# Kernel optimization log

Measured on AMD Instinct MI355X. Metric: run time of the kernel, lower is better.

## Reference

```python
import jax, jax.numpy as jnp
import numpy as np

B, T, D = 2, 2048, 2048
H, DK = 16, 96
DV = 192                 # head_v_dim = head_dim * expand_v (expand_v=2)
KEY_DIM = H * DK         # 1536 = 0.75*D
VAL_DIM = H * DV         # 3072 = 1.5*D
KS = 4                   # short-conv kernel size
EPS = 1e-6


def setup_inputs() -> dict:
    key = jax.random.key(0)
    ks = jax.random.split(key, 16)
    nrm = lambda k, shape, s: jax.random.normal(k, shape, jnp.float32) * s
    # dt_bias init as in the torch module
    dt_min, dt_max = 1e-3, 1e-1
    dt = jnp.exp(jax.random.uniform(ks[12], (H,), jnp.float32)
                 * (np.log(dt_max) - np.log(dt_min)) + np.log(dt_min))
    dt_bias = dt + jnp.log(-jnp.expm1(-dt))
    return {
        'x': nrm(ks[0], (B, T, D), 1.0),
        'Wq': nrm(ks[1], (D, KEY_DIM), D ** -0.5),
        'Wk': nrm(ks[2], (D, KEY_DIM), D ** -0.5),
        'Wv': nrm(ks[3], (D, VAL_DIM), D ** -0.5),
        'Wb': nrm(ks[4], (D, H), D ** -0.5),
        'Wa': nrm(ks[5], (D, H), D ** -0.5),
        'Wg': nrm(ks[6], (D, VAL_DIM), D ** -0.5),
        'Wo': nrm(ks[7], (VAL_DIM, D), VAL_DIM ** -0.5),
        'conv_q_w': nrm(ks[8], (KEY_DIM, KS), KS ** -0.5),
        'conv_k_w': nrm(ks[9], (KEY_DIM, KS), KS ** -0.5),
        'conv_v_w': nrm(ks[10], (VAL_DIM, KS), KS ** -0.5),
        'A_log': jnp.log(jax.random.uniform(ks[11], (H,), jnp.float32, 1e-4, 16.0)),
        'dt_bias': dt_bias,
        'o_norm_weight': jnp.ones((DV,), jnp.float32),
    }


def _causal_depthwise_conv(x, w):
    # x: (B, T, C), w: (C, KS). Depthwise causal conv + SiLU.
    xp = jnp.pad(x, ((0, 0), (KS - 1, 0), (0, 0)))
    y = sum(xp[:, j:j + T, :] * w[:, j] for j in range(KS))
    return jax.nn.silu(y)


def _gated_delta_scan(q, k, v, g, beta):
    # q,k: (B,T,H,DK)  v: (B,T,H,DV)  g,beta: (B,T,H)
    def step(S, inp):
        q_t, k_t, v_t, g_t, b_t = inp          # (B,H,DK),(B,H,DK),(B,H,DV),(B,H),(B,H)
        alpha = jnp.exp(g_t)                   # (B,H)
        retrieved = jnp.einsum('bhk,bhkv->bhv', k_t, S)
        error = v_t - retrieved                # (B,H,DV)
        S = alpha[:, :, None, None] * S + b_t[:, :, None, None] * (
            k_t[:, :, :, None] * error[:, :, None, :])
        o_t = jnp.einsum('bhk,bhkv->bhv', q_t, S)
        return S, o_t

    tm = lambda a: jnp.swapaxes(a, 0, 1)       # time-major
    S0 = jnp.zeros((B, H, DK, DV), jnp.float32)
    _, o = jax.lax.scan(step, S0, (tm(q), tm(k), tm(v), tm(g), tm(beta)))
    return jnp.swapaxes(o, 0, 1)               # (B,T,H,DV)


def reference(x, Wq, Wk, Wv, Wb, Wa, Wg, Wo,
              conv_q_w, conv_k_w, conv_v_w, A_log, dt_bias, o_norm_weight):
    # projections + causal depthwise short conv + SiLU
    q = _causal_depthwise_conv(x @ Wq, conv_q_w).reshape(B, T, H, DK)
    k = _causal_depthwise_conv(x @ Wk, conv_k_w).reshape(B, T, H, DK)
    v = _causal_depthwise_conv(x @ Wv, conv_v_w).reshape(B, T, H, DV)

    beta = jax.nn.sigmoid(x @ Wb)                                   # (B,T,H)
    g = -jnp.exp(A_log) * jax.nn.softplus(x @ Wa + dt_bias)         # (B,T,H)

    # qk L2 normalization (use_qk_l2norm_in_kernel=True path)
    q = q * jax.lax.rsqrt(jnp.sum(q * q, -1, keepdims=True) + 1e-12)
    k = k * jax.lax.rsqrt(jnp.sum(k * k, -1, keepdims=True) + 1e-12)

    o = _gated_delta_scan(q, k, v, g, beta)                         # (B,T,H,DV)

    # gated RMSNorm over head_v_dim
    g_out = (x @ Wg).reshape(B, T, H, DV)
    rms = jax.lax.rsqrt(jnp.mean(o * o, -1, keepdims=True) + EPS)
    o = (o * rms) * o_norm_weight * jax.nn.sigmoid(g_out)

    return o.reshape(B, T, VAL_DIM) @ Wo                            # (B,T,D)
```

## Files before the change

kernel.cpp:

```cpp
#include <hip/hip_runtime.h>

#define B_ 2
#define T_ 2048
#define D_ 2048
#define H_ 16
#define DK_ 96
#define DV_ 192
#define KEYD 1536
#define VALD 3072
#define NPROJ 9216
#define PQK 6144
#define KS_ 4
#define C_ 64
#define NC_ 32

typedef unsigned short u16;
typedef unsigned int u32;
typedef __bf16 bf16x8 __attribute__((ext_vector_type(8)));
typedef float f32x4 __attribute__((ext_vector_type(4)));

__device__ __forceinline__ u16 f2bf(float f) {
  unsigned u = __float_as_uint(f);
  u += 0x7FFF + ((u >> 16) & 1);
  return (u16)(u >> 16);
}
__device__ __forceinline__ float bf2f(u16 v) { return __uint_as_float((unsigned)v << 16); }
__device__ __forceinline__ float bflo(u32 w) { return __uint_as_float(w << 16); }
__device__ __forceinline__ float bfhi(u32 w) { return __uint_as_float(w & 0xFFFF0000u); }

__device__ __forceinline__ void gll16(const void* g, void* lds) {
  __builtin_amdgcn_global_load_lds(
      (const __attribute__((address_space(1))) void*)g,
      (__attribute__((address_space(3))) void*)lds, 16, 0, 0);
}

__global__ __launch_bounds__(256) void cast_x(const float* __restrict__ in,
                                              u16* __restrict__ out, int n4) {
  int i = blockIdx.x * 256 + threadIdx.x;
  if (i < n4) {
    float4 v = reinterpret_cast<const float4*>(in)[i];
    ushort4 o;
    o.x = f2bf(v.x); o.y = f2bf(v.y); o.z = f2bf(v.z); o.w = f2bf(v.w);
    reinterpret_cast<ushort4*>(out)[i] = o;
  }
}

__global__ __launch_bounds__(256) void transpose_cast(const float* __restrict__ src,
                                                      u16* __restrict__ dst, int R, int C) {
  __shared__ float tile[32][33];
  int tx = threadIdx.x & 31, ty = threadIdx.x >> 5;
  int c0 = blockIdx.x * 32, r0 = blockIdx.y * 32;
#pragma unroll
  for (int j = 0; j < 4; ++j)
    tile[ty + j * 8][tx] = src[(size_t)(r0 + ty + j * 8) * C + c0 + tx];
  __syncthreads();
#pragma unroll
  for (int j = 0; j < 4; ++j)
    dst[(size_t)(c0 + ty + j * 8) * R + r0 + tx] = f2bf(tile[tx][ty + j * 8]);
}

template <int OUT16>
__global__ __launch_bounds__(512, 2) void gemm256(const u16* __restrict__ A,
    const u16* __restrict__ BT, u16* __restrict__ C0, u16* __restrict__ C1,
    float* __restrict__ Cf, int M, int N, int K, int nsplit, int s0, int s1) {
  __shared__ u16 LA[2][256 * 64];
  __shared__ u16 LB[2][256 * 64];
  const int tid = threadIdx.x, wave = tid >> 6, lane = tid & 63;
  const int l15 = lane & 15, l16 = lane >> 4, x7 = l15 & 7;
  const int wr = wave >> 2, wc = wave & 3;
  const int m0 = blockIdx.y * 256, n0 = blockIdx.x * 256;
  const int r8 = lane >> 3;
  const int csrc = ((lane & 7) ^ r8) << 3;
  const int NKT = K >> 6;
  f32x4 acc[8][4] = {};

#define STG_A(p, kt, half) { \
    const u16* As_ = A + (size_t)m0 * K + (size_t)(kt) * 64; \
    _Pragma("unroll") \
    for (int g = 0; g < 2; ++g) { \
      int rowb = g * 128 + (half) * 64 + wave * 8; \
      gll16(As_ + (size_t)(rowb + r8) * K + csrc, (char*)&LA[p][0] + rowb * 128); \
    } \
  }
#define STG_B(p, kt) { \
    const u16* Bs_ = BT + (size_t)n0 * K + (size_t)(kt) * 64; \
    _Pragma("unroll") \
    for (int j = 0; j < 4; ++j) { \
      int rowb = j * 64 + wave * 8; \
      gll16(Bs_ + (size_t)(rowb + r8) * K + csrc, (char*)&LB[p][0] + rowb * 128); \
    } \
  }

#define LDA8(p, mh, dst) { \
    _Pragma("unroll") \
    for (int mi = 0; mi < 4; ++mi) \
      _Pragma("unroll") \
      for (int kk = 0; kk < 2; ++kk) { \
        int row = wr * 128 + (mh) * 64 + mi * 16 + l15; \
        dst[mi * 2 + kk] = *(const bf16x8*)((const char*)&LA[p][0] + row * 128 + (((kk * 4 + l16) ^ x7) << 4)); \
      } \
  }
#define LDB4(p, nh, dst) { \
    _Pragma("unroll") \
    for (int ni = 0; ni < 2; ++ni) \
      _Pragma("unroll") \
      for (int kk = 0; kk < 2; ++kk) { \
        int row = wc * 64 + (nh) * 32 + ni * 16 + l15; \
        dst[ni * 2 + kk] = *(const bf16x8*)((const char*)&LB[p][0] + row * 128 + (((kk * 4 + l16) ^ x7) << 4)); \
      } \
  }

#define MMQ(AF, BF, mbase, nbase) { \
    __builtin_amdgcn_s_setprio(1); \
    _Pragma("unroll") \
    for (int mi = 0; mi < 4; ++mi) \
      _Pragma("unroll") \
      for (int ni = 0; ni < 2; ++ni) \
        _Pragma("unroll") \
        for (int kk = 0; kk < 2; ++kk) \
          acc[(mbase) + mi][(nbase) + ni] = __builtin_amdgcn_mfma_f32_16x16x32_bf16( \
              AF[mi * 2 + kk], BF[ni * 2 + kk], acc[(mbase) + mi][(nbase) + ni], 0, 0, 0); \
    __builtin_amdgcn_s_setprio(0); \
  }

#define BARR() __builtin_amdgcn_s_barrier()
#define LGKM0() { asm volatile("s_waitcnt lgkmcnt(0)" ::: "memory"); __builtin_amdgcn_sched_barrier(0); }

  STG_A(0, 0, 0); STG_A(0, 0, 1); STG_B(0, 0);
  if (NKT > 1) {
    STG_A(1, 1, 0); STG_A(1, 1, 1); STG_B(1, 1);
    asm volatile("s_waitcnt vmcnt(8)" ::: "memory");
  } else {
    asm volatile("s_waitcnt vmcnt(0)" ::: "memory");
  }
  BARR();

  bf16x8 afA[8], afB[8], bf0[4], bf1[4];
  for (int c = 0; c < NKT; ++c) {
    const int p = c & 1;
    const bool stg = (c + 2 < NKT);
    LDA8(p, 0, afA); LDB4(p, 0, bf0);
    BARR();
    LGKM0();
    MMQ(afA, bf0, 0, 0);
    BARR();
    LDB4(p, 1, bf1);
    if (stg) STG_A(p, c + 2, 0);
    BARR();
    LGKM0();
    MMQ(afA, bf1, 0, 2);
    BARR();
    LDA8(p, 1, afB);
    if (stg) STG_B(p, c + 2);
    BARR();
    LGKM0();
    MMQ(afB, bf1, 4, 2);
    BARR();
    if (stg) {
      STG_A(p, c + 2, 1);
      asm volatile("s_waitcnt vmcnt(8)" ::: "memory");
    } else if (c + 1 < NKT) {
      asm volatile("s_waitcnt vmcnt(0)" ::: "memory");
    }
    BARR();
    MMQ(afB, bf0, 4, 0);
    BARR();
  }

#pragma unroll
  for (int mi = 0; mi < 8; ++mi)
#pragma unroll
    for (int ni = 0; ni < 4; ++ni)
#pragma unroll
      for (int j = 0; j < 4; ++j) {
        int row = m0 + wr * 128 + mi * 16 + l16 * 4 + j;
        int col = n0 + wc * 64 + ni * 16 + l15;
        float v = acc[mi][ni][j];
        if (OUT16) {
          if (col < nsplit) C0[(size_t)row * s0 + col] = f2bf(v);
          else              C1[(size_t)row * s1 + col - nsplit] = f2bf(v);
        } else {
          Cf[(size_t)row * N + col] = v;
        }
      }
#undef STG_A
#undef STG_B
#undef LDA8
#undef LDB4
#undef MMQ
#undef BARR
#undef LGKM0
}

template <int OUT16>
__global__ __launch_bounds__(256) void gemm_bt(const u16* __restrict__ A,
                                               const u16* __restrict__ BT,
                                               u16* __restrict__ C0, u16* __restrict__ C1,
                                               float* __restrict__ Cf,
                                               int M, int N, int K, int nsplit, int s0, int s1) {
  __shared__ u16 As[128 * 32];
  __shared__ u16 Bs[128 * 32];
  int tid = threadIdx.x;
  int wave = tid >> 6, lane = tid & 63;
  int l15 = lane & 15, l16 = lane >> 4;
  int m0 = blockIdx.y * 128, n0 = blockIdx.x * 128;
  int wm = (wave >> 1) * 64, wn = (wave & 1) * 64;
  f32x4 acc[4][4] = {};
  int nkt = K >> 5;
  for (int kt = 0; kt < nkt; ++kt) {
    int k0 = kt << 5;
    __syncthreads();
#pragma unroll
    for (int rr = 0; rr < 2; ++rr) {
      int idx = tid + rr * 256;
      int row = idx >> 2, kc8 = (idx & 3) * 8;
      unsigned loff = (unsigned)(rr * 256 + wave * 64) * 16;
      gll16(A + (size_t)(m0 + row) * K + k0 + kc8, (char*)As + loff);
      gll16(BT + (size_t)(n0 + row) * K + k0 + kc8, (char*)Bs + loff);
    }
    __syncthreads();
    bf16x8 af[4], bfr[4];
#pragma unroll
    for (int i = 0; i < 4; ++i)
      af[i] = *reinterpret_cast<const bf16x8*>(&As[(wm + i * 16 + l15) * 32 + l16 * 8]);
#pragma unroll
    for (int i = 0; i < 4; ++i)
      bfr[i] = *reinterpret_cast<const bf16x8*>(&Bs[(wn + i * 16 + l15) * 32 + l16 * 8]);
#pragma unroll
    for (int mi = 0; mi < 4; ++mi)
#pragma unroll
      for (int ni = 0; ni < 4; ++ni)
        acc[mi][ni] = __builtin_amdgcn_mfma_f32_16x16x32_bf16(af[mi], bfr[ni], acc[mi][ni], 0, 0, 0);
  }
#pragma unroll
  for (int mi = 0; mi < 4; ++mi)
#pragma unroll
    for (int ni = 0; ni < 4; ++ni)
#pragma unroll
      for (int j = 0; j < 4; ++j) {
        int row = m0 + wm + mi * 16 + l16 * 4 + j;
        int col = n0 + wn + ni * 16 + l15;
        if (OUT16) {
          if (col < nsplit) C0[(size_t)row * s0 + col] = f2bf(acc[mi][ni][j]);
          else              C1[(size_t)row * s1 + col - nsplit] = f2bf(acc[mi][ni][j]);
        } else {
          Cf[(size_t)row * N + col] = acc[mi][ni][j];
        }
      }
}

__global__ __launch_bounds__(256) void proj_bg(const float* __restrict__ x,
    const float* __restrict__ Wb, const float* __restrict__ Wa,
    const float* __restrict__ A_log, const float* __restrict__ dt_bias,
    float* __restrict__ beta, float* __restrict__ gg) {
  __shared__ float xs[4 * 2048];
  __shared__ float red[4][32][8];
  int tid = threadIdx.x;
  int r0 = blockIdx.x * 4;
  for (int i = tid; i < 4 * 2048; i += 256)
    xs[i] = x[(size_t)r0 * D_ + i];
  __syncthreads();
  int colg = tid & 31, ks = tid >> 5;
  const float* W = (colg < 16) ? Wb : Wa;
  int wc = colg & 15;
  float p0 = 0, p1 = 0, p2 = 0, p3 = 0;
  int kbeg = ks * 256;
  for (int k = kbeg; k < kbeg + 256; ++k) {
    float wv = W[k * H_ + wc];
    p0 += xs[k] * wv;
    p1 += xs[2048 + k] * wv;
    p2 += xs[4096 + k] * wv;
    p3 += xs[6144 + k] * wv;
  }
  red[0][colg][ks] = p0; red[1][colg][ks] = p1;
  red[2][colg][ks] = p2; red[3][colg][ks] = p3;
  __syncthreads();
  if (tid < 128) {
    int row = tid >> 5, col = tid & 31;
    float d = 0;
#pragma unroll
    for (int i = 0; i < 8; ++i) d += red[row][col][i];
    int r = r0 + row;
    if (col < 16) {
      beta[(size_t)r * H_ + col] = 1.f / (1.f + __expf(-d));
    } else {
      int hh = col - 16;
      float z = d + dt_bias[hh];
      float sp = (z > 20.f) ? z : log1pf(__expf(z));
      gg[(size_t)r * H_ + hh] = -__expf(A_log[hh]) * sp;
    }
  }
}

__global__ __launch_bounds__(256) void conv_qkv(const u16* __restrict__ Pqkv,
    const float* __restrict__ wq, const float* __restrict__ wk, const float* __restrict__ wv,
    u16* __restrict__ qc, u16* __restrict__ kc, u16* __restrict__ vc) {
  int bt = blockIdx.x;
  int t = bt & (T_ - 1);
  int tid = threadIdx.x, h = tid >> 4, li = tid & 15;
#pragma unroll
  for (int part = 0; part < 2; ++part) {
    const float* w = part ? wk : wq;
    const u16* base = Pqkv + (size_t)bt * PQK + part * KEYD + h * DK_;
    float y[6]; float ss = 0.f;
#pragma unroll
    for (int jj = 0; jj < 6; ++jj) {
      int c = li + jj * 16;
      int ch = h * DK_ + c;
      float a = 0.f;
#pragma unroll
      for (int j = 0; j < KS_; ++j) {
        int dt = j - (KS_ - 1);
        if (t + dt >= 0) a += bf2f(base[(ptrdiff_t)dt * PQK + c]) * w[ch * KS_ + j];
      }
      float yv = a / (1.f + __expf(-a));
      y[jj] = yv; ss += yv * yv;
    }
    ss += __shfl_xor(ss, 1); ss += __shfl_xor(ss, 2);
    ss += __shfl_xor(ss, 4); ss += __shfl_xor(ss, 8);
    float rn = rsqrtf(ss + 1e-12f);
    u16* out = (part ? kc : qc) + (size_t)bt * KEYD + h * DK_;
#pragma unroll
    for (int jj = 0; jj < 6; ++jj) out[li + jj * 16] = f2bf(y[jj] * rn);
  }
  const u16* vbase = Pqkv + (size_t)bt * PQK + 2 * KEYD;
  u16* vout = vc + (size_t)bt * VALD;
#pragma unroll
  for (int jj = 0; jj < 12; ++jj) {
    int c = tid + jj * 256;
    float a = 0.f;
#pragma unroll
    for (int j = 0; j < KS_; ++j) {
      int dt = j - (KS_ - 1);
      if (t + dt >= 0) a += bf2f(vbase[(ptrdiff_t)dt * PQK + c]) * wv[c * KS_ + j];
    }
    vout[c] = f2bf(a / (1.f + __expf(-a)));
  }
}

__global__ __launch_bounds__(320) void chunk_prep(
    const u16* __restrict__ kc, u16* __restrict__ Uv ,
    const float* __restrict__ gg, const float* __restrict__ beta,
    u16* __restrict__ Wg, float* __restrict__ Gcum,
    float* __restrict__ cdArr, float* __restrict__ lamArr) {
  __shared__ __align__(16) u16 ktL[64 * 104];
  __shared__ float AmL[64 * 68];
  __shared__ float glL[64], GclL[64], blL[64], DplL[64];
  int tid = threadIdx.x;
  int flat = blockIdx.x;
  int c = flat & 31, bh = flat >> 5, h = bh & 15, b = bh >> 4;
  int bT0 = b * T_ + c * 64;

  {
    const u32* kg = (const u32*)(kc + (size_t)bT0 * KEYD + h * DK_);
    for (int i = tid; i < 3072; i += 320) {
      int t = i / 48, dd = i - t * 48;
      ((u32*)ktL)[t * 52 + dd] = kg[(size_t)t * (KEYD / 2) + dd];
    }
  }
  if (tid < 64) {
    float g = gg[(size_t)(bT0 + tid) * H_ + h];
    float bv = beta[(size_t)(bT0 + tid) * H_ + h];
    float v = g;
#pragma unroll
    for (int off = 1; off < 64; off <<= 1) {
      float u = __shfl_up(v, off);
      if (tid >= off) v += u;
    }
    float g63 = __shfl(v, 63);
    glL[tid] = g; GclL[tid] = v; blL[tid] = bv; DplL[tid] = __expf(v - g);
    Gcum[(size_t)flat * 64 + tid] = v;
    cdArr[(size_t)flat * 64 + tid] = bv * __expf(g63 - v);
    if (tid == 63) lamArr[flat] = __expf(v);
  }
  __syncthreads();

  {
    int wave = tid >> 6, lane = tid & 63, l15 = lane & 15, l16 = lane >> 4;
    if (wave < 4) {
      f32x4 ac[4] = {};
#pragma unroll
      for (int ks = 0; ks < 3; ++ks) {
        bf16x8 a = *(const bf16x8*)&ktL[(wave * 16 + l15) * 104 + ks * 32 + l16 * 8];
#pragma unroll
        for (int n = 0; n < 4; ++n) {
          bf16x8 bb = *(const bf16x8*)&ktL[(n * 16 + l15) * 104 + ks * 32 + l16 * 8];
          ac[n] = __builtin_amdgcn_mfma_f32_16x16x32_bf16(a, bb, ac[n], 0, 0, 0);
        }
      }
#pragma unroll
      for (int n = 0; n < 4; ++n)
#pragma unroll
        for (int j = 0; j < 4; ++j) {
          int t = wave * 16 + l16 * 4 + j;
          int jj = n * 16 + l15;
          float val = 0.f;
          if (jj < t) val = __expf((GclL[t] - glL[t]) - GclL[jj]) * blL[jj] * ac[n][j];
          AmL[t * 68 + jj] = val;
        }
    }
  }
  __syncthreads();

  if (tid < 288) {
    int j = tid;
    float m[64];
    if (j < 192) {
      const u16* up = Uv + (size_t)bT0 * VALD + h * DV_ + j;
#pragma unroll
      for (int t = 0; t < 64; ++t) m[t] = bf2f(up[(size_t)t * VALD]);
    } else {
      int d = j - 192;
#pragma unroll
      for (int t = 0; t < 64; ++t) m[t] = DplL[t] * bf2f(ktL[t * 104 + d]);
    }
#pragma unroll
    for (int t0 = 0; t0 < 64; t0 += 4) {
      {
        f32x4 a1 = *(const f32x4*)&AmL[(t0 + 1) * 68 + t0];
        m[t0 + 1] -= a1[0] * m[t0];
        f32x4 a2 = *(const f32x4*)&AmL[(t0 + 2) * 68 + t0];
        m[t0 + 2] -= a2[0] * m[t0] + a2[1] * m[t0 + 1];
        f32x4 a3 = *(const f32x4*)&AmL[(t0 + 3) * 68 + t0];
        m[t0 + 3] -= a3[0] * m[t0] + a3[1] * m[t0 + 1] + a3[2] * m[t0 + 2];
      }
#pragma unroll
      for (int tp = t0 + 4; tp < 64; ++tp) {
        f32x4 a = *(const f32x4*)&AmL[tp * 68 + t0];
        m[tp] -= a[0] * m[t0] + a[1] * m[t0 + 1] + a[2] * m[t0 + 2] + a[3] * m[t0 + 3];
      }
    }
    if (j < 192) {
      u16* up = Uv + (size_t)bT0 * VALD + h * DV_ + j;
#pragma unroll
      for (int t = 0; t < 64; ++t) up[(size_t)t * VALD] = f2bf(m[t]);
    } else {
      int d = j - 192;
      u16* wp = Wg + (size_t)bT0 * KEYD + h * DK_ + d;
#pragma unroll
      for (int t = 0; t < 64; ++t) wp[(size_t)t * KEYD] = f2bf(m[t]);
    }
  }
}

__global__ __launch_bounds__(256) void serial_state(
    const u16* __restrict__ kc, const u16* __restrict__ Wg, u16* __restrict__ Ue,
    const float* __restrict__ cdArr, const float* __restrict__ lamArr,
    u16* __restrict__ Schk) {
  __shared__ __align__(16) u16 WtL[2][64 * 104];
  __shared__ __align__(16) u16 ktT[2][96 * 72];
  __shared__ __align__(16) u16 StH[32 * 104];
  __shared__ __align__(16) u16 StLo[32 * 104];
  __shared__ __align__(16) u16 EtH[32 * 72];
  __shared__ __align__(16) u16 EtLo[32 * 72];
  __shared__ float lamS[2];

  int tid = threadIdx.x, wave = tid >> 6, lane = tid & 63;
  int l15 = lane & 15, l16 = lane >> 4;
  int jq = blockIdx.x % 6, bh = blockIdx.x / 6, h = bh & 15, b = bh >> 4;
  int col0 = jq * 32;
  int ntS = wave & 1, m3 = 3 * (wave >> 1);
  int st_t = tid >> 2, st_dd = (tid & 3) * 12;

  f32x4 Sf[3] = {};
  uint4 wreg[3], kreg[3];
  u16 ureg[2][4];
  float cdv[4];
  float lamReg;

#define PREFETCH(bT0p, flatp) { \
    const u32* wgp = (const u32*)(Wg + (size_t)((bT0p) + st_t) * KEYD + h * DK_) + st_dd; \
    const u32* kgp = (const u32*)(kc + (size_t)((bT0p) + st_t) * KEYD + h * DK_) + st_dd; \
    wreg[0] = ((const uint4*)wgp)[0]; wreg[1] = ((const uint4*)wgp)[1]; wreg[2] = ((const uint4*)wgp)[2]; \
    kreg[0] = ((const uint4*)kgp)[0]; kreg[1] = ((const uint4*)kgp)[1]; kreg[2] = ((const uint4*)kgp)[2]; \
    _Pragma("unroll") \
    for (int ni = 0; ni < 2; ++ni) \
      _Pragma("unroll") \
      for (int j = 0; j < 4; ++j) \
        ureg[ni][j] = Ue[(size_t)((bT0p) + wave * 16 + l16 * 4 + j) * VALD + h * DV_ + col0 + ni * 16 + l15]; \
    _Pragma("unroll") \
    for (int j = 0; j < 4; ++j) cdv[j] = cdArr[(size_t)(flatp) * 64 + wave * 16 + l16 * 4 + j]; \
    if (tid == 0) lamReg = lamArr[flatp]; \
  }

  PREFETCH(b * T_, bh * NC_);

  for (int c = 0; c < NC_; ++c) {
    int buf = c & 1;
    int flat = bh * NC_ + c;
    int bT0 = b * T_ + (c << 6);
    {
      u32* wl = (u32*)&WtL[buf][0] + st_t * 52 + st_dd;
      ((uint4*)wl)[0] = wreg[0];
      *(uint4*)(wl + 4) = wreg[1];
      *(uint4*)(wl + 8) = wreg[2];
#pragma unroll
      for (int r = 0; r < 3; ++r) {
        u32 vals[4] = {kreg[r].x, kreg[r].y, kreg[r].z, kreg[r].w};
#pragma unroll
        for (int e = 0; e < 4; ++e) {
          int d = 2 * (st_dd + r * 4 + e);
          ktT[buf][d * 72 + st_t] = (u16)(vals[e] & 0xFFFFu);
          ktT[buf][(d + 1) * 72 + st_t] = (u16)(vals[e] >> 16);
        }
      }
      int cl = ntS * 16 + l15;
      u16* schkRow = Schk + (size_t)flat * (DK_ * DV_) + (size_t)(col0 + cl) * DK_;
#pragma unroll
      for (int i = 0; i < 3; ++i) {
        u16 hi0 = f2bf(Sf[i][0]), hi1 = f2bf(Sf[i][1]);
        u16 hi2 = f2bf(Sf[i][2]), hi3 = f2bf(Sf[i][3]);
        int dbase = (m3 + i) * 16 + l16 * 4;
        StH[cl * 104 + dbase + 0] = hi0; StLo[cl * 104 + dbase + 0] = f2bf(Sf[i][0] - bf2f(hi0));
        StH[cl * 104 + dbase + 1] = hi1; StLo[cl * 104 + dbase + 1] = f2bf(Sf[i][1] - bf2f(hi1));
        StH[cl * 104 + dbase + 2] = hi2; StLo[cl * 104 + dbase + 2] = f2bf(Sf[i][2] - bf2f(hi2));
        StH[cl * 104 + dbase + 3] = hi3; StLo[cl * 104 + dbase + 3] = f2bf(Sf[i][3] - bf2f(hi3));
        u32* ow = (u32*)(schkRow + dbase);
        ow[0] = ((u32)hi1 << 16) | hi0;
        ow[1] = ((u32)hi3 << 16) | hi2;
      }
      if (tid == 0) lamS[buf] = lamReg;
    }
    __syncthreads();
    {
      f32x4 Ea[2] = {};
#pragma unroll
      for (int ks = 0; ks < 3; ++ks) {
        bf16x8 a = *(const bf16x8*)&WtL[buf][(wave * 16 + l15) * 104 + ks * 32 + l16 * 8];
#pragma unroll
        for (int ni = 0; ni < 2; ++ni) {
          bf16x8 bhv = *(const bf16x8*)&StH[(ni * 16 + l15) * 104 + ks * 32 + l16 * 8];
          bf16x8 blv = *(const bf16x8*)&StLo[(ni * 16 + l15) * 104 + ks * 32 + l16 * 8];
          Ea[ni] = __builtin_amdgcn_mfma_f32_16x16x32_bf16(a, bhv, Ea[ni], 0, 0, 0);
          Ea[ni] = __builtin_amdgcn_mfma_f32_16x16x32_bf16(a, blv, Ea[ni], 0, 0, 0);
        }
      }
#pragma unroll
      for (int ni = 0; ni < 2; ++ni)
#pragma unroll
        for (int j = 0; j < 4; ++j) {
          int t = wave * 16 + l16 * 4 + j;
          float ev = bf2f(ureg[ni][j]) - Ea[ni][j];
          Ue[(size_t)(bT0 + t) * VALD + h * DV_ + col0 + ni * 16 + l15] = f2bf(ev);
          float ep = cdv[j] * ev;
          u16 ehi = f2bf(ep);
          int cl = ni * 16 + l15;
          EtH[cl * 72 + t] = ehi;
          EtLo[cl * 72 + t] = f2bf(ep - bf2f(ehi));
        }
      if (c + 1 < NC_) PREFETCH(bT0 + 64, flat + 1);
    }
    __syncthreads();
    {
      float lam = lamS[buf];
#pragma unroll
      for (int i = 0; i < 3; ++i)
#pragma unroll
        for (int j = 0; j < 4; ++j) Sf[i][j] *= lam;
#pragma unroll
      for (int ks = 0; ks < 2; ++ks) {
        bf16x8 bhv = *(const bf16x8*)&EtH[(ntS * 16 + l15) * 72 + ks * 32 + l16 * 8];
        bf16x8 blv = *(const bf16x8*)&EtLo[(ntS * 16 + l15) * 72 + ks * 32 + l16 * 8];
#pragma unroll
        for (int i = 0; i < 3; ++i) {
          bf16x8 a = *(const bf16x8*)&ktT[buf][((m3 + i) * 16 + l15) * 72 + ks * 32 + l16 * 8];
          Sf[i] = __builtin_amdgcn_mfma_f32_16x16x32_bf16(a, bhv, Sf[i], 0, 0, 0);
          Sf[i] = __builtin_amdgcn_mfma_f32_16x16x32_bf16(a, blv, Sf[i], 0, 0, 0);
        }
      }
    }
  }
#undef PREFETCH
}

__global__ __launch_bounds__(256) void chunk_out(
    const u16* __restrict__ qc, const u16* __restrict__ kc, const u16* __restrict__ Ee,
    const u16* __restrict__ Schk, const float* __restrict__ Gcum,
    const float* __restrict__ beta, u16* __restrict__ osc) {
  __shared__ __align__(16) char pool[65280];
  u16* qL   = (u16*)pool;
  u16* BmL  = (u16*)(pool + 12288);
  u16* BmLo = (u16*)(pool + 21504);
  u16* kL   = (u16*)(pool + 30720);
  u16* StL  = (u16*)(pool + 30720);
  u16* EtL  = (u16*)(pool + 50688);
  float* GclL = (float*)(pool + 64512);
  float* blL  = (float*)(pool + 64768);
  float* DlL  = (float*)(pool + 65024);

  int tid = threadIdx.x, wave = tid >> 6, lane = tid & 63;
  int l15 = lane & 15, l16 = lane >> 4;
  int flat = blockIdx.x;
  int c = flat & 31, bh = flat >> 5, h = bh & 15, b = bh >> 4;
  int bT0 = b * T_ + c * 64;

  {
    const u32* qg = (const u32*)(qc + (size_t)bT0 * KEYD + h * DK_);
    const u32* kg = (const u32*)(kc + (size_t)bT0 * KEYD + h * DK_);
    for (int i = tid; i < 3072; i += 256) {
      int t = i / 48, dd = i - t * 48;
      ((u32*)qL)[t * 48 + dd] = qg[(size_t)t * (KEYD / 2) + dd];
      ((u32*)kL)[t * 48 + dd] = kg[(size_t)t * (KEYD / 2) + dd];
    }
    if (tid < 64) {
      float gv = Gcum[(size_t)flat * 64 + tid];
      GclL[tid] = gv;
      DlL[tid] = __expf(gv);
      blL[tid] = beta[(size_t)(bT0 + tid) * H_ + h];
    }
  }
  __syncthreads();

  {
    f32x4 bacc[4] = {};
#pragma unroll
    for (int kk = 0; kk < 3; ++kk) {
      bf16x8 aq = *(const bf16x8*)&qL[(wave * 16 + l15) * 96 + kk * 32 + l16 * 8];
#pragma unroll
      for (int n = 0; n < 4; ++n) {
        bf16x8 bk = *(const bf16x8*)&kL[(n * 16 + l15) * 96 + kk * 32 + l16 * 8];
        bacc[n] = __builtin_amdgcn_mfma_f32_16x16x32_bf16(aq, bk, bacc[n], 0, 0, 0);
      }
    }
#pragma unroll
    for (int n = 0; n < 4; ++n)
#pragma unroll
      for (int j = 0; j < 4; ++j) {
        int t = wave * 16 + l16 * 4 + j;
        int jj = n * 16 + l15;
        float val = 0.f;
        if (jj <= t) val = __expf(GclL[t] - GclL[jj]) * blL[jj] * bacc[n][j];
        u16 hi = f2bf(val);
        BmL[t * 72 + jj] = hi;
        BmLo[t * 72 + jj] = f2bf(val - bf2f(hi));
      }
  }
  __syncthreads();

#pragma unroll
  for (int half = 0; half < 2; ++half) {
    {
      const u32* sg = (const u32*)(Schk + (size_t)flat * (DK_ * DV_) + (size_t)(half * 96) * DK_);
      for (int i = tid; i < 4608; i += 256) {
        int cL = i / 48, dd = i - cL * 48;
        ((u32*)&StL[cL * 104])[dd] = sg[cL * 48 + dd];
      }
      const u32* eg = (const u32*)(Ee + (size_t)bT0 * VALD + h * DV_ + half * 96);
      for (int i = tid; i < 3072; i += 256) {
        int t = i / 48, dd = i - t * 48;
        u32 w2 = eg[(size_t)t * (VALD / 2) + dd];
        EtL[(2 * dd) * 72 + t]     = (u16)(w2 & 0xFFFF);
        EtL[(2 * dd + 1) * 72 + t] = (u16)(w2 >> 16);
      }
    }
    __syncthreads();
    f32x4 oacc[6] = {};
#pragma unroll
    for (int kk = 0; kk < 3; ++kk) {
      bf16x8 aq = *(const bf16x8*)&qL[(wave * 16 + l15) * 96 + kk * 32 + l16 * 8];
#pragma unroll
      for (int n = 0; n < 6; ++n) {
        bf16x8 bs = *(const bf16x8*)&StL[(n * 16 + l15) * 104 + kk * 32 + l16 * 8];
        oacc[n] = __builtin_amdgcn_mfma_f32_16x16x32_bf16(aq, bs, oacc[n], 0, 0, 0);
      }
    }
#pragma unroll
    for (int n = 0; n < 6; ++n)
#pragma unroll
      for (int j = 0; j < 4; ++j)
        oacc[n][j] *= DlL[wave * 16 + l16 * 4 + j];
#pragma unroll
    for (int kk = 0; kk < 2; ++kk) {
      bf16x8 ah = *(const bf16x8*)&BmL[(wave * 16 + l15) * 72 + kk * 32 + l16 * 8];
      bf16x8 al = *(const bf16x8*)&BmLo[(wave * 16 + l15) * 72 + kk * 32 + l16 * 8];
#pragma unroll
      for (int n = 0; n < 6; ++n) {
        bf16x8 be = *(const bf16x8*)&EtL[(n * 16 + l15) * 72 + kk * 32 + l16 * 8];
        oacc[n] = __builtin_amdgcn_mfma_f32_16x16x32_bf16(ah, be, oacc[n], 0, 0, 0);
        oacc[n] = __builtin_amdgcn_mfma_f32_16x16x32_bf16(al, be, oacc[n], 0, 0, 0);
      }
    }
#pragma unroll
    for (int n = 0; n < 6; ++n)
#pragma unroll
      for (int j = 0; j < 4; ++j) {
        int t = wave * 16 + l16 * 4 + j;
        int cc = half * 96 + n * 16 + l15;
        osc[(size_t)(bT0 + t) * VALD + h * DV_ + cc] = f2bf(oacc[n][j]);
      }
    __syncthreads();
  }
}

__global__ __launch_bounds__(256) void rmsnorm_gate(const u16* __restrict__ o,
    const u16* __restrict__ Pg, const float* __restrict__ w, u16* __restrict__ onb) {
  int bt = blockIdx.x;
  int tid = threadIdx.x, h = tid >> 4, li = tid & 15;
  const u16* orow = o + (size_t)bt * VALD + h * DV_;
  const u16* grow = Pg + (size_t)bt * VALD + h * DV_;
  float y[12]; float ss = 0.f;
#pragma unroll
  for (int jj = 0; jj < 12; ++jj) {
    float v = bf2f(orow[li + jj * 16]);
    y[jj] = v; ss += v * v;
  }
  ss += __shfl_xor(ss, 1); ss += __shfl_xor(ss, 2);
  ss += __shfl_xor(ss, 4); ss += __shfl_xor(ss, 8);
  float rms = rsqrtf(ss * (1.f / DV_) + 1e-6f);
  u16* out = onb + (size_t)bt * VALD + h * DV_;
#pragma unroll
  for (int jj = 0; jj < 12; ++jj) {
    int c = li + jj * 16;
    float gv = bf2f(grow[c]);
    float sig = 1.f / (1.f + __expf(-gv));
    out[c] = f2bf(y[jj] * rms * w[c] * sig);
  }
}

extern "C" void kernel_launch(void* const* d_in, const int* in_sizes, int n_in,
                              void* d_out, int out_size, void* d_ws, size_t ws_size,
                              hipStream_t stream) {
  (void)in_sizes; (void)n_in; (void)out_size; (void)ws_size;
  const float* x      = (const float*)d_in[0];
  const float* Wq     = (const float*)d_in[1];
  const float* Wk     = (const float*)d_in[2];
  const float* Wv     = (const float*)d_in[3];
  const float* Wb     = (const float*)d_in[4];
  const float* Wa     = (const float*)d_in[5];
  const float* Wg     = (const float*)d_in[6];
  const float* Wo     = (const float*)d_in[7];
  const float* cqw    = (const float*)d_in[8];
  const float* ckw    = (const float*)d_in[9];
  const float* cvw    = (const float*)d_in[10];
  const float* A_log  = (const float*)d_in[11];
  const float* dt_bias= (const float*)d_in[12];
  const float* onw    = (const float*)d_in[13];
  float* out = (float*)d_out;

  char* ws = (char*)d_ws;
  u16*   xb    = (u16*)  (ws + 0);
  u16*   WT    = (u16*)  (ws + 16777216);
  u16*   qc    = (u16*)  (ws + 0);
  u16*   kc    = (u16*)  (ws + 12582912);
  u16*   vc    = (u16*)  (ws + 25165824);
  u16*   Pqkv  = (u16*)  (ws + 54525952);
  u16*   Wbuf  = (u16*)  (ws + 54525952);
  u16*   Schk  = (u16*)  (ws + 67108864);
  u16*   Pg    = (u16*)  (ws + 104857600);
  u16*   osc   = (u16*)  (ws + 130023424);
  float* beta  = (float*)(ws + 155189248);
  float* gg    = (float*)(ws + 155451392);
  float* Gcum  = (float*)(ws + 155713536);
  float* cdArr = (float*)(ws + 155975680);
  float* lamArr= (float*)(ws + 156237824);
  u16*   onb   = (u16*)  (ws + 54525952);
  u16*   WoT   = (u16*)  (ws + 79691776);

  int n4 = B_ * T_ * D_ / 4;
  cast_x<<<(n4 + 255) / 256, 256, 0, stream>>>(x, xb, n4);
  transpose_cast<<<dim3(48, 64), 256, 0, stream>>>(Wq, WT, 2048, 1536);
  transpose_cast<<<dim3(48, 64), 256, 0, stream>>>(Wk, WT + (size_t)1536 * 2048, 2048, 1536);
  transpose_cast<<<dim3(96, 64), 256, 0, stream>>>(Wv, WT + (size_t)3072 * 2048, 2048, 3072);
  transpose_cast<<<dim3(96, 64), 256, 0, stream>>>(Wg, WT + (size_t)6144 * 2048, 2048, 3072);

  gemm256<1><<<dim3(NPROJ / 256, (B_ * T_) / 256), 512, 0, stream>>>(
      xb, WT, Pqkv, Pg, nullptr, B_ * T_, NPROJ, D_, PQK, PQK, VALD);
  proj_bg<<<(B_ * T_) / 4, 256, 0, stream>>>(x, Wb, Wa, A_log, dt_bias, beta, gg);
  conv_qkv<<<B_ * T_, 256, 0, stream>>>(Pqkv, cqw, ckw, cvw, qc, kc, vc);

  chunk_prep<<<B_ * H_ * NC_, 320, 0, stream>>>(kc, vc, gg, beta, Wbuf, Gcum, cdArr, lamArr);
  serial_state<<<B_ * H_ * 6, 256, 0, stream>>>(kc, Wbuf, vc, cdArr, lamArr, Schk);
  chunk_out<<<B_ * H_ * NC_, 256, 0, stream>>>(qc, kc, vc, Schk, Gcum, beta, osc);

  rmsnorm_gate<<<B_ * T_, 256, 0, stream>>>(osc, Pg, onw, onb);
  transpose_cast<<<dim3(64, 96), 256, 0, stream>>>(Wo, WoT, 3072, 2048);
  gemm_bt<0><<<dim3(D_ / 128, (B_ * T_) / 128), 256, 0, stream>>>(
      onb, WoT, nullptr, nullptr, out, B_ * T_, D_, VALD, 0, 0, 0);
}
```

Measured before the change: 631.3 us.

## Fuse gated RMSNorm into chunk_out, stage conv rows in LDS, drop GEMM lgkm waits

The gated RMSNorm epilogue moves into chunk_out: both output halves stay in registers, Pg and the norm weight are staged in shared memory, and the normalised, gated result is written straight to onb. This removes the osc round-trip through global memory and one kernel launch. conv_qkv now loads the four needed Pqkv rows into shared memory once instead of doing repeated scattered global reads. The explicit lgkmcnt(0) waits in the 256-tile GEMM are also removed, leaving the compiler to insert LDS waits, which could change scheduling or correctness ordering; keeping two accumulator sets raises register pressure in chunk_out.

```diff
diff --git a/kernel.cpp b/kernel.cpp
--- a/kernel.cpp
+++ b/kernel.cpp
@@ -124,7 +124,6 @@
   }
 
 #define BARR() __builtin_amdgcn_s_barrier()
-#define LGKM0() { asm volatile("s_waitcnt lgkmcnt(0)" ::: "memory"); __builtin_amdgcn_sched_barrier(0); }
 
   STG_A(0, 0, 0); STG_A(0, 0, 1); STG_B(0, 0);
   if (NKT > 1) {
@@ -141,19 +140,16 @@
     const bool stg = (c + 2 < NKT);
     LDA8(p, 0, afA); LDB4(p, 0, bf0);
     BARR();
-    LGKM0();
     MMQ(afA, bf0, 0, 0);
     BARR();
     LDB4(p, 1, bf1);
     if (stg) STG_A(p, c + 2, 0);
     BARR();
-    LGKM0();
     MMQ(afA, bf1, 0, 2);
     BARR();
     LDA8(p, 1, afB);
     if (stg) STG_B(p, c + 2);
     BARR();
-    LGKM0();
     MMQ(afB, bf1, 4, 2);
     BARR();
     if (stg) {
@@ -189,7 +185,6 @@
 #undef LDB4
 #undef MMQ
 #undef BARR
-#undef LGKM0
 }
 
 template <int OUT16>
@@ -295,13 +290,29 @@
 __global__ __launch_bounds__(256) void conv_qkv(const u16* __restrict__ Pqkv,
     const float* __restrict__ wq, const float* __restrict__ wk, const float* __restrict__ wv,
     u16* __restrict__ qc, u16* __restrict__ kc, u16* __restrict__ vc) {
+  __shared__ __align__(16) u16 rows[4][PQK];
   int bt = blockIdx.x;
   int t = bt & (T_ - 1);
   int tid = threadIdx.x, h = tid >> 4, li = tid & 15;
 #pragma unroll
+  for (int r = 0; r < 4; ++r) {
+    bool valid = (t + r - 3) >= 0;
+    const uint4* src = (const uint4*)(Pqkv + (ptrdiff_t)(bt + r - 3) * PQK);
+    uint4* dst = (uint4*)rows[r];
+#pragma unroll
+    for (int i = 0; i < 3; ++i) {
+      int off = tid + i * 256;
+      uint4 v;
+      if (valid) v = src[off];
+      else { v.x = 0; v.y = 0; v.z = 0; v.w = 0; }
+      dst[off] = v;
+    }
+  }
+  __syncthreads();
+
+#pragma unroll
   for (int part = 0; part < 2; ++part) {
     const float* w = part ? wk : wq;
-    const u16* base = Pqkv + (size_t)bt * PQK + part * KEYD + h * DK_;
     float y[6]; float ss = 0.f;
 #pragma unroll
     for (int jj = 0; jj < 6; ++jj) {
@@ -309,10 +320,8 @@
       int ch = h * DK_ + c;
       float a = 0.f;
 #pragma unroll
-      for (int j = 0; j < KS_; ++j) {
-        int dt = j - (KS_ - 1);
-        if (t + dt >= 0) a += bf2f(base[(ptrdiff_t)dt * PQK + c]) * w[ch * KS_ + j];
-      }
+      for (int j = 0; j < KS_; ++j)
+        a += bf2f(rows[j][part * KEYD + ch]) * w[ch * KS_ + j];
       float yv = a / (1.f + __expf(-a));
       y[jj] = yv; ss += yv * yv;
     }
@@ -323,17 +332,14 @@
 #pragma unroll
     for (int jj = 0; jj < 6; ++jj) out[li + jj * 16] = f2bf(y[jj] * rn);
   }
-  const u16* vbase = Pqkv + (size_t)bt * PQK + 2 * KEYD;
   u16* vout = vc + (size_t)bt * VALD;
 #pragma unroll
   for (int jj = 0; jj < 12; ++jj) {
     int c = tid + jj * 256;
     float a = 0.f;
 #pragma unroll
-    for (int j = 0; j < KS_; ++j) {
-      int dt = j - (KS_ - 1);
-      if (t + dt >= 0) a += bf2f(vbase[(ptrdiff_t)dt * PQK + c]) * wv[c * KS_ + j];
-    }
+    for (int j = 0; j < KS_; ++j)
+      a += bf2f(rows[j][2 * KEYD + c]) * wv[c * KS_ + j];
     vout[c] = f2bf(a / (1.f + __expf(-a)));
   }
 }
@@ -576,7 +582,8 @@
 __global__ __launch_bounds__(256) void chunk_out(
     const u16* __restrict__ qc, const u16* __restrict__ kc, const u16* __restrict__ Ee,
     const u16* __restrict__ Schk, const float* __restrict__ Gcum,
-    const float* __restrict__ beta, u16* __restrict__ osc) {
+    const float* __restrict__ beta, const u16* __restrict__ Pg,
+    const float* __restrict__ onw, u16* __restrict__ onb) {
   __shared__ __align__(16) char pool[65280];
   u16* qL   = (u16*)pool;
   u16* BmL  = (u16*)(pool + 12288);
@@ -587,6 +594,8 @@
   float* GclL = (float*)(pool + 64512);
   float* blL  = (float*)(pool + 64768);
   float* DlL  = (float*)(pool + 65024);
+  u16* PgL  = (u16*)pool;
+  float* wL = (float*)(pool + 24576);
 
   int tid = threadIdx.x, wave = tid >> 6, lane = tid & 63;
   int l15 = lane & 15, l16 = lane >> 4;
@@ -637,84 +646,103 @@
   }
   __syncthreads();
 
-#pragma unroll
-  for (int half = 0; half < 2; ++half) {
-    {
-      const u32* sg = (const u32*)(Schk + (size_t)flat * (DK_ * DV_) + (size_t)(half * 96) * DK_);
-      for (int i = tid; i < 4608; i += 256) {
-        int cL = i / 48, dd = i - cL * 48;
-        ((u32*)&StL[cL * 104])[dd] = sg[cL * 48 + dd];
-      }
-      const u32* eg = (const u32*)(Ee + (size_t)bT0 * VALD + h * DV_ + half * 96);
-      for (int i = tid; i < 3072; i += 256) {
-        int t = i / 48, dd = i - t * 48;
-        u32 w2 = eg[(size_t)t * (VALD / 2) + dd];
-        EtL[(2 * dd) * 72 + t]     = (u16)(w2 & 0xFFFF);
-        EtL[(2 * dd + 1) * 72 + t] = (u16)(w2 >> 16);
-      }
-    }
-    __syncthreads();
-    f32x4 oacc[6] = {};
-#pragma unroll
-    for (int kk = 0; kk < 3; ++kk) {
-      bf16x8 aq = *(const bf16x8*)&qL[(wave * 16 + l15) * 96 + kk * 32 + l16 * 8];
-#pragma unroll
-      for (int n = 0; n < 6; ++n) {
-        bf16x8 bs = *(const bf16x8*)&StL[(n * 16 + l15) * 104 + kk * 32 + l16 * 8];
-        oacc[n] = __builtin_amdgcn_mfma_f32_16x16x32_bf16(aq, bs, oacc[n], 0, 0, 0);
-      }
-    }
-#pragma unroll
-    for (int n = 0; n < 6; ++n)
-#pragma unroll
-      for (int j = 0; j < 4; ++j)
-        oacc[n][j] *= DlL[wave * 16 + l16 * 4 + j];
-#pragma unroll
-    for (int kk = 0; kk < 2; ++kk) {
-      bf16x8 ah = *(const bf16x8*)&BmL[(wave * 16 + l15) * 72 + kk * 32 + l16 * 8];
-      bf16x8 al = *(const bf16x8*)&BmLo[(wave * 16 + l15) * 72 + kk * 32 + l16 * 8];
-#pragma unroll
-      for (int n = 0; n < 6; ++n) {
-        bf16x8 be = *(const bf16x8*)&EtL[(n * 16 + l15) * 72 + kk * 32 + l16 * 8];
-        oacc[n] = __builtin_amdgcn_mfma_f32_16x16x32_bf16(ah, be, oacc[n], 0, 0, 0);
-        oacc[n] = __builtin_amdgcn_mfma_f32_16x16x32_bf16(al, be, oacc[n], 0, 0, 0);
-      }
-    }
-#pragma unroll
-    for (int n = 0; n < 6; ++n)
-#pragma unroll
-      for (int j = 0; j < 4; ++j) {
-        int t = wave * 16 + l16 * 4 + j;
-        int cc = half * 96 + n * 16 + l15;
-        osc[(size_t)(bT0 + t) * VALD + h * DV_ + cc] = f2bf(oacc[n][j]);
-      }
-    __syncthreads();
-  }
-}
-
-__global__ __launch_bounds__(256) void rmsnorm_gate(const u16* __restrict__ o,
-    const u16* __restrict__ Pg, const float* __restrict__ w, u16* __restrict__ onb) {
-  int bt = blockIdx.x;
-  int tid = threadIdx.x, h = tid >> 4, li = tid & 15;
-  const u16* orow = o + (size_t)bt * VALD + h * DV_;
-  const u16* grow = Pg + (size_t)bt * VALD + h * DV_;
-  float y[12]; float ss = 0.f;
-#pragma unroll
-  for (int jj = 0; jj < 12; ++jj) {
-    float v = bf2f(orow[li + jj * 16]);
-    y[jj] = v; ss += v * v;
-  }
-  ss += __shfl_xor(ss, 1); ss += __shfl_xor(ss, 2);
-  ss += __shfl_xor(ss, 4); ss += __shfl_xor(ss, 8);
-  float rms = rsqrtf(ss * (1.f / DV_) + 1e-6f);
-  u16* out = onb + (size_t)bt * VALD + h * DV_;
-#pragma unroll
-  for (int jj = 0; jj < 12; ++jj) {
-    int c = li + jj * 16;
-    float gv = bf2f(grow[c]);
-    float sig = 1.f / (1.f + __expf(-gv));
-    out[c] = f2bf(y[jj] * rms * w[c] * sig);
-  }
+  f32x4 oacc0[6] = {};
+  f32x4 oacc1[6] = {};
+
+#define HALFC(half, OACC) { \
+    { \
+      const u32* sg = (const u32*)(Schk + (size_t)flat * (DK_ * DV_) + (size_t)((half) * 96) * DK_); \
+      for (int i = tid; i < 4608; i += 256) { \
+        int cL = i / 48, dd = i - cL * 48; \
+        ((u32*)&StL[cL * 104])[dd] = sg[cL * 48 + dd]; \
+      } \
+      const u32* eg = (const u32*)(Ee + (size_t)bT0 * VALD + h * DV_ + (half) * 96); \
+      for (int i = tid; i < 3072; i += 256) { \
+        int t = i / 48, dd = i - t * 48; \
+        u32 w2 = eg[(size_t)t * (VALD / 2) + dd]; \
+        EtL[(2 * dd) * 72 + t]     = (u16)(w2 & 0xFFFF); \
+        EtL[(2 * dd + 1) * 72 + t] = (u16)(w2 >> 16); \
+      } \
+    } \
+    __syncthreads(); \
+    _Pragma("unroll") \
+    for (int kk = 0; kk < 3; ++kk) { \
+      bf16x8 aq = *(const bf16x8*)&qL[(wave * 16 + l15) * 96 + kk * 32 + l16 * 8]; \
+      _Pragma("unroll") \
+      for (int n = 0; n < 6; ++n) { \
+        bf16x8 bs = *(const bf16x8*)&StL[(n * 16 + l15) * 104 + kk * 32 + l16 * 8]; \
+        OACC[n] = __builtin_amdgcn_mfma_f32_16x16x32_bf16(aq, bs, OACC[n], 0, 0, 0); \
+      } \
+    } \
+    _Pragma("unroll") \
+    for (int n = 0; n < 6; ++n) \
+      _Pragma("unroll") \
+      for (int j = 0; j < 4; ++j) \
+        OACC[n][j] *= DlL[wave * 16 + l16 * 4 + j]; \
+    _Pragma("unroll") \
+    for (int kk = 0; kk < 2; ++kk) { \
+      bf16x8 ah = *(const bf16x8*)&BmL[(wave * 16 + l15) * 72 + kk * 32 + l16 * 8]; \
+      bf16x8 al = *(const bf16x8*)&BmLo[(wave * 16 + l15) * 72 + kk * 32 + l16 * 8]; \
+      _Pragma("unroll") \
+      for (int n = 0; n < 6; ++n) { \
+        bf16x8 be = *(const bf16x8*)&EtL[(n * 16 + l15) * 72 + kk * 32 + l16 * 8]; \
+        OACC[n] = __builtin_amdgcn_mfma_f32_16x16x32_bf16(ah, be, OACC[n], 0, 0, 0); \
+        OACC[n] = __builtin_amdgcn_mfma_f32_16x16x32_bf16(al, be, OACC[n], 0, 0, 0); \
+      } \
+    } \
+    __syncthreads(); \
+  }
+
+  HALFC(0, oacc0);
+  HALFC(1, oacc1);
+#undef HALFC
+
+  {
+    const uint4* pgg = (const uint4*)(Pg + (size_t)bT0 * VALD + h * DV_);
+    int tr = tid >> 2, q = tid & 3;
+    uint4* dstRow = (uint4*)&PgL[tr * 192];
+    const uint4* srcRow = (const uint4*)((const u16*)pgg + (size_t)tr * VALD);
+#pragma unroll
+    for (int ii = 0; ii < 6; ++ii)
+      dstRow[q * 6 + ii] = srcRow[q * 6 + ii];
+    if (tid < 192) wL[tid] = onw[tid];
+  }
+  __syncthreads();
+
+  float ssv[4] = {0.f, 0.f, 0.f, 0.f};
+#pragma unroll
+  for (int n = 0; n < 6; ++n)
+#pragma unroll
+    for (int j = 0; j < 4; ++j) {
+      float y0 = bf2f(f2bf(oacc0[n][j]));
+      float y1 = bf2f(f2bf(oacc1[n][j]));
+      ssv[j] += y0 * y0 + y1 * y1;
+    }
+#pragma unroll
+  for (int j = 0; j < 4; ++j) {
+    ssv[j] += __shfl_xor(ssv[j], 1); ssv[j] += __shfl_xor(ssv[j], 2);
+    ssv[j] += __shfl_xor(ssv[j], 4); ssv[j] += __shfl_xor(ssv[j], 8);
+  }
+  float rmsv[4];
+#pragma unroll
+  for (int j = 0; j < 4; ++j) rmsv[j] = rsqrtf(ssv[j] * (1.f / DV_) + 1e-6f);
+
+#define EPIL(OACC, half) { \
+    _Pragma("unroll") \
+    for (int n = 0; n < 6; ++n) \
+      _Pragma("unroll") \
+      for (int j = 0; j < 4; ++j) { \
+        int t = wave * 16 + l16 * 4 + j; \
+        int cc = (half) * 96 + n * 16 + l15; \
+        float yv = bf2f(f2bf(OACC[n][j])); \
+        float gv = bf2f(PgL[t * 192 + cc]); \
+        float sig = 1.f / (1.f + __expf(-gv)); \
+        onb[(size_t)(bT0 + t) * VALD + h * DV_ + cc] = f2bf(yv * rmsv[j] * wL[cc] * sig); \
+      } \
+  }
+  EPIL(oacc0, 0);
+  EPIL(oacc1, 1);
+#undef EPIL
 }
 
 extern "C" void kernel_launch(void* const* d_in, const int* in_sizes, int n_in,
@@ -747,7 +775,6 @@
   u16*   Wbuf  = (u16*)  (ws + 54525952);
   u16*   Schk  = (u16*)  (ws + 67108864);
   u16*   Pg    = (u16*)  (ws + 104857600);
-  u16*   osc   = (u16*)  (ws + 130023424);
   float* beta  = (float*)(ws + 155189248);
   float* gg    = (float*)(ws + 155451392);
   float* Gcum  = (float*)(ws + 155713536);
@@ -770,9 +797,8 @@
 
   chunk_prep<<<B_ * H_ * NC_, 320, 0, stream>>>(kc, vc, gg, beta, Wbuf, Gcum, cdArr, lamArr);
   serial_state<<<B_ * H_ * 6, 256, 0, stream>>>(kc, Wbuf, vc, cdArr, lamArr, Schk);
-  chunk_out<<<B_ * H_ * NC_, 256, 0, stream>>>(qc, kc, vc, Schk, Gcum, beta, osc);
-
-  rmsnorm_gate<<<B_ * T_, 256, 0, stream>>>(osc, Pg, onw, onb);
+  chunk_out<<<B_ * H_ * NC_, 256, 0, stream>>>(qc, kc, vc, Schk, Gcum, beta, Pg, onw, onb);
+
   transpose_cast<<<dim3(64, 96), 256, 0, stream>>>(Wo, WoT, 3072, 2048);
   gemm_bt<0><<<dim3(D_ / 128, (B_ * T_) / 128), 256, 0, stream>>>(
       onb, WoT, nullptr, nullptr, out, B_ * T_, D_, VALD, 0, 0, 0);
```

New measurement: 567.9 us. -10.0%, faster.
